# Kernel tuning notes

Hardware: AMD Instinct MI355X
Metric: run time of the kernel (lower is better)

## Reference

```python
import jax, jax.numpy as jnp
from jax import lax
import numpy as np

D_IN = 12      # latent_dim / flow input_dim
HALF = 6       # coupling split
HID = 192      # flow_hidden_dim
LAYERS = 24    # flow_layers
N_BASES = 66
SYM = 12       # symmetry_dim
OUT_DIM = 6    # rows of tangent frame J_p
B = 16384
EPS_P = 1e-3
CLAMP = 2.0    # soft clamp for 'exp_clamp' scale map: s = CLAMP*tanh(raw/CLAMP)


def _mlp(z1, p):
    W1, b1, W2, b2, W3, b3 = p
    h = jax.nn.relu(z1 @ W1.T + b1)
    h = jax.nn.relu(h @ W2.T + b2)
    return h @ W3.T + b3


def _coupling_fwd(z, p):
    # AffineCouplingBlock (split->affine->merge) followed by Permute(swap)
    z1, z2 = z[..., :HALF], z[..., HALF:]
    prm = _mlp(z1, p)
    shift, sraw = prm[..., 0::2], prm[..., 1::2]
    s = CLAMP * jnp.tanh(sraw / CLAMP)
    z2 = z2 * jnp.exp(s) + shift
    # merge [z1, z2'] then swap halves -> [z2', z1]
    return jnp.concatenate([z2, z1], axis=-1), jnp.sum(s, axis=-1)


def _coupling_inv(z, p):
    # inverse of Permute(swap) is swap again
    z = jnp.concatenate([z[..., HALF:], z[..., :HALF]], axis=-1)
    z1, z2 = z[..., :HALF], z[..., HALF:]
    prm = _mlp(z1, p)
    shift, sraw = prm[..., 0::2], prm[..., 1::2]
    s = CLAMP * jnp.tanh(sraw / CLAMP)
    z2 = (z2 - shift) * jnp.exp(-s)
    return jnp.concatenate([z1, z2], axis=-1), -jnp.sum(s, axis=-1)


def flow_forward(z, params):
    def step(c, p):
        z, ld = c
        z, d = _coupling_fwd(z, p)
        return (z, ld + d), None
    (z, ld), _ = lax.scan(step, (z, jnp.zeros(z.shape[:-1], z.dtype)), params)
    return z, ld


def flow_inverse(y, params):
    def step(c, p):
        z, ld = c
        z, d = _coupling_inv(z, p)
        return (z, ld + d), None
    (z, ld), _ = lax.scan(step, (y, jnp.zeros(y.shape[:-1], y.dtype)), params, reverse=True)
    return z, ld


def pullback_tangent(z, v, params):
    # J[b] = v[b] @ d(flow_forward)/dz at z[b], via per-sample vjp
    def one(zb, vb):
        _, vjp_fn = jax.vjp(lambda zz: flow_forward(zz, params)[0], zb)
        return jax.vmap(lambda r: vjp_fn(r)[0])(vb)
    return jax.vmap(one)(z, v)


def kl_divergence(J_p, J_q, log_var_diag):
    b, out_dim, in_dim = J_p.shape
    J_p = J_p / jnp.sqrt(jnp.sum(J_p * J_p))  # global normalization
    S_p = jnp.einsum('bni,bmi->bnm', J_p, J_p)
    S_q = jnp.einsum('bin,bim->bnm', J_q, J_q)
    S_pq = jnp.einsum('bni,bmi->bnm', J_p[:, :, :SYM], J_q)
    D = jnp.exp(-log_var_diag)  # (in_dim,)
    I_p = jnp.eye(out_dim, dtype=J_p.dtype)
    I_q = jnp.eye(SYM, dtype=J_q.dtype)
    M = S_p + EPS_P * I_p
    H = S_q + D[:SYM] * I_q
    norm_M = jnp.maximum(jnp.mean(jnp.diagonal(M, axis1=-2, axis2=-1), -1), 1e-6)
    norm_H = jnp.maximum(jnp.mean(jnp.diagonal(H, axis1=-2, axis2=-1), -1), 1e-6)
    M = M + 1e-3 * norm_M[:, None, None] * I_p
    H = H + 1e-3 * norm_H[:, None, None] * I_q
    Db = D + 1e-3 * norm_H[:, None]  # (b, in_dim)
    trace_p = jnp.einsum('bij,bij,bj->b', J_p, J_p, Db)
    trace_q = jnp.einsum('bij,bij->b', J_q, J_q)
    trace_pq = jnp.einsum('bij,bij->b', S_pq, S_pq)
    trace = (EPS_P + 1e-3 * norm_M) * (jnp.sum(Db, -1) + trace_q) + trace_p + trace_pq
    L_M = jnp.linalg.cholesky(M)
    L_H = jnp.linalg.cholesky(H)
    logdet_M = 2.0 * jnp.sum(jnp.log(jnp.diagonal(L_M, axis1=-2, axis2=-1)), -1)
    logdet_H = 2.0 * jnp.sum(jnp.log(jnp.diagonal(L_H, axis1=-2, axis2=-1)), -1)
    logdet_p = logdet_M + (in_dim - out_dim) * np.float32(np.log(EPS_P))
    logdet_q = logdet_H + jnp.sum(jnp.log(Db[:, SYM:]), -1)
    logdet = -(logdet_p + logdet_q)
    return 0.5 * (trace + logdet - in_dim)


def setup_inputs() -> dict:
    key = jax.random.key(0)
    ks = jax.random.split(key, 10)
    y = jax.random.normal(ks[0], (B, D_IN), jnp.float32)
    J_p = jax.random.normal(ks[1], (B, OUT_DIM, D_IN), jnp.float32)
    sc = 0.05
    W1 = sc * jax.random.normal(ks[2], (LAYERS, HID, HALF), jnp.float32)
    b1 = sc * jax.random.normal(ks[3], (LAYERS, HID), jnp.float32)
    W2 = sc * jax.random.normal(ks[4], (LAYERS, HID, HID), jnp.float32)
    b2 = sc * jax.random.normal(ks[5], (LAYERS, HID), jnp.float32)
    W3 = sc * jax.random.normal(ks[6], (LAYERS, D_IN, HID), jnp.float32)
    b3 = sc * jax.random.normal(ks[7], (LAYERS, D_IN), jnp.float32)
    Wsym = (1.0 / np.sqrt(SYM)) * jax.random.normal(ks[8], (N_BASES, SYM, SYM), jnp.float32)
    log_var_diag = jnp.zeros((D_IN,), jnp.float32)
    return {"y": y, "J_p": J_p, "W1": W1, "b1": b1, "W2": W2, "b2": b2,
            "W3": W3, "b3": b3, "Wsym": Wsym, "log_var_diag": log_var_diag}


def reference(y, J_p, W1, b1, W2, b2, W3, b3, Wsym, log_var_diag):
    params = (W1, b1, W2, b2, W3, b3)
    z, ld = flow_inverse(y, params)
    # DiagGaussian(trainable=False) base log prob = standard normal
    log_prob = ld - 0.5 * D_IN * np.float32(np.log(2.0 * np.pi)) - 0.5 * jnp.sum(z * z, -1)
    Jp = pullback_tangent(z, J_p, params)
    A = Wsym - jnp.swapaxes(Wsym, -1, -2)
    J_q = jnp.einsum('bi,mji->bmj', z[:, :SYM], A)
    kl = kl_divergence(Jp, J_q, log_var_diag)
    return (log_prob, kl)
```

## Files before the change

### kernel.cpp

```cpp
#include <hip/hip_runtime.h>
#include <hip/hip_bf16.h>
#include <math.h>

#define BTOT   16384
#define NLAYER 24
#define NDIN   12
#define HID    192
#define NBASE  66
#define EPSP   1e-3f
#define EPB    16

#define EST 200
#define W3ST 12
#define OB_H1  0
#define OB_G   6400
#define OB_R   44800
#define OB_W1  49408
#define OB_W3F 51712
#define OB_PRM 60928
#define OB_GZ  61696
#define OB_ZAB 64000
#define OB_ES  65536
#define OB_LD  65920
#define OB_ZQ  65984
#define OB_RED 66048
#define SMEM_BYTES 66080

typedef __attribute__((ext_vector_type(8))) short s8v;
typedef __attribute__((ext_vector_type(4))) float f4v;
#define MFMA16(a,b,c) __builtin_amdgcn_mfma_f32_16x16x32_bf16(a,b,c,0,0,0)

__device__ __forceinline__ unsigned short f2bf(float f) {
  unsigned u = __builtin_bit_cast(unsigned, f);
  u += 0x7fffu + ((u >> 16) & 1u);
  return (unsigned short)(u >> 16);
}
__device__ __forceinline__ float bf2f(unsigned short h) {
  unsigned u = ((unsigned)h) << 16;
  return __builtin_bit_cast(float, u);
}
__device__ __forceinline__ unsigned pk2(float a, float b) {
  return (unsigned)f2bf(a) | ((unsigned)f2bf(b) << 16);
}
__device__ __forceinline__ float blo(unsigned u) { return bf2f((unsigned short)(u & 0xffff)); }
__device__ __forceinline__ float bhi(unsigned u) { return bf2f((unsigned short)(u >> 16)); }

__global__ void prep_kernel(const float* __restrict__ W2,
                            unsigned short* __restrict__ w2b,
                            unsigned short* __restrict__ w2t) {
  int idx = blockIdx.x * 256 + threadIdx.x;
  int l   = idx / (HID * HID);
  int rem = idx - l * HID * HID;
  int k   = rem / HID;
  int j   = rem - k * HID;
  w2b[idx] = f2bf(W2[idx]);
  w2t[idx] = f2bf(W2[l * HID * HID + j * HID + k]);
}

__global__ __launch_bounds__(256) void flow_kernel(
    float* __restrict__ yz, float* __restrict__ jp,
    const float* __restrict__ W1, const float* __restrict__ b1,
    const float* __restrict__ b2,
    const float* __restrict__ W3, const float* __restrict__ b3,
    const unsigned short* __restrict__ w2b,
    const unsigned short* __restrict__ w2t,
    float* __restrict__ ws_sum, float* __restrict__ out_lp) {
  extern __shared__ char smraw[];
  unsigned short* sH1b = (unsigned short*)(smraw + OB_H1);
  unsigned short* sGb  = (unsigned short*)(smraw + OB_G);
  float* sW3f = (float*)(smraw + OB_W3F);
  float* sR   = (float*)(smraw + OB_R);
  float* cur  = (float*)(smraw + OB_PRM);
  float* sGZ  = (float*)(smraw + OB_GZ);
  float* sZA  = (float*)(smraw + OB_ZAB);
  float* sZB  = sZA + 192;
  float* sES  = (float*)(smraw + OB_ES);
  float* sLD  = (float*)(smraw + OB_LD);
  float* sZQ  = (float*)(smraw + OB_ZQ);
  float* sRed = (float*)(smraw + OB_RED);

  const int tid  = threadIdx.x;
  const int lane = tid & 63;
  const int w    = __builtin_amdgcn_readfirstlane(tid >> 6);
  const int e    = tid & 15;
  const int grp  = tid >> 4;
  const int lm   = lane & 15, lq = lane >> 4;
  const int blk  = blockIdx.x;

  if (tid < 96) {
    int i = tid >> 4;
    sZA[96 + i * 16 + e] = yz[(blk * EPB + e) * 12 + i];
    sZB[96 + i * 16 + e] = yz[(blk * EPB + e) * 12 + 6 + i];
  }
  if (tid < 16) { sLD[tid] = 0.f; sZQ[tid] = 0.f; }
  if (tid == 0) sRed[0] = 0.f;
  for (int idx = tid; idx < 576; idx += 256) sGZ[idx] = 0.f;
  for (int idx = tid; idx < 72 * EPB; idx += 256) {
    int rt = idx >> 4, ee = idx & 15;
    sR[idx] = jp[(blk * EPB + ee) * 72 + rt];
  }
  __syncthreads();

  for (int l = NLAYER - 1; l >= 0; --l) {
    const float* W1l = W1 + l * HID * 6;
    const float* b1l = b1 + l * HID;
    const float* b2l = b2 + l * HID;
    const float* W3l = W3 + l * NDIN * HID;
    const float* b3l = b3 + l * NDIN;
    const unsigned short* w2bl = w2b + l * HID * HID;
    const unsigned short* w2tl = w2t + l * HID * HID;
    const int p = l & 1;

    if (tid < 192) {
      const float* wr = W1l + tid * 6;
      unsigned* dst = (unsigned*)(smraw + OB_W1 + tid * 12);
      dst[0] = pk2(wr[0], wr[1]);
      dst[1] = pk2(wr[2], wr[3]);
      dst[2] = pk2(wr[4], wr[5]);
    }
    for (int idx = tid; idx < 2304; idx += 256) {
      int t = idx / 192, j = idx - t * 192;
      sW3f[j * W3ST + t] = W3l[idx];
    }
    if (tid < 192) cur[tid] = 0.f;
    if (l != NLAYER - 1) {
      for (int idx = tid; idx < 576; idx += 256) {
        int i = idx / 96, rem = idx - i * 96;
        int r = rem >> 4, e5 = rem & 15;
        float r1  = sR[(r * 12 + i) * EPB + e5];
        float r2o = sR[(r * 12 + 6 + i) * EPB + e5];
        float es  = sES[i * 16 + e5];
        sR[(r * 12 + i) * EPB + e5]     = r2o + sGZ[i * 96 + rem];
        sR[(r * 12 + 6 + i) * EPB + e5] = r1 * es;
        sGZ[i * 96 + rem] = 0.f;
      }
    }
    {
      float z1v[6];
      #pragma unroll
      for (int i = 0; i < 6; ++i) z1v[i] = sZB[p * 96 + i * 16 + e];
      #pragma unroll
      for (int ch = 0; ch < 2; ++ch) {
        int j0 = grp * 12 + ch * 6;
        float hv[6];
        #pragma unroll
        for (int jj = 0; jj < 6; ++jj) {
          int j = j0 + jj;
          float acc = b1l[j];
          #pragma unroll
          for (int i = 0; i < 6; ++i) acc = fmaf(W1l[j * 6 + i], z1v[i], acc);
          hv[jj] = fmaxf(acc, 0.f);
        }
        unsigned* dst = (unsigned*)&sH1b[e * EST + j0];
        dst[0] = pk2(hv[0], hv[1]);
        dst[1] = pk2(hv[2], hv[3]);
        dst[2] = pk2(hv[4], hv[5]);
      }
    }
    __syncthreads();

    {
      f4v acc2[3] = {{0,0,0,0},{0,0,0,0},{0,0,0,0}};
      #pragma unroll 2
      for (int kk = 0; kk < 6; ++kk) {
        int jo = kk * 32 + lq * 8;
        s8v Bv = *(const s8v*)&sH1b[lm * EST + jo];
        #pragma unroll
        for (int s = 0; s < 3; ++s) {
          s8v A = *(const s8v*)(w2bl + ((w + s * 4) * 16 + lm) * HID + jo);
          acc2[s] = MFMA16(A, Bv, acc2[s]);
        }
      }
      #pragma unroll
      for (int s = 0; s < 3; ++s) {
        int jb2 = (w + s * 4) * 16 + lq * 4;
        float hv[4];
        #pragma unroll
        for (int rg = 0; rg < 4; ++rg)
          hv[rg] = fmaxf(acc2[s][rg] + b2l[jb2 + rg], 0.f);
        unsigned* dst = (unsigned*)sGb + ((lm * EST + jb2) >> 1);
        dst[0] = pk2(hv[0], hv[1]);
        dst[1] = pk2(hv[2], hv[3]);
        float pp[12];
        #pragma unroll
        for (int t = 0; t < 12; ++t) pp[t] = 0.f;
        #pragma unroll
        for (int rg = 0; rg < 4; ++rg) {
          const float* w3r = sW3f + (jb2 + rg) * W3ST;
          float v = hv[rg];
          #pragma unroll
          for (int t = 0; t < 12; ++t) pp[t] = fmaf(w3r[t], v, pp[t]);
        }
        #pragma unroll
        for (int t = 0; t < 12; ++t) {
          float v = pp[t];
          v += __shfl_xor(v, 16);
          v += __shfl_xor(v, 32);
          if (lane < 16) atomicAdd(&cur[t * EPB + lane], v);
        }
      }
    }
    __syncthreads();

    {
      unsigned mbits = 0;
      {
        const unsigned* hp = (const unsigned*)&sGb[e * EST + grp * 12];
        #pragma unroll
        for (int c = 0; c < 6; ++c) {
          unsigned m = hp[c];
          mbits |= ((m & 0xffffu) ? 1u : 0u) << (2 * c);
          mbits |= ((m >> 16)     ? 1u : 0u) << (2 * c + 1);
        }
      }
      float tf[6];
      #pragma unroll
      for (int c = 0; c < 6; ++c) {
        float sh = b3l[2 * c]     + cur[(2 * c) * EPB + e];
        float sr = b3l[2 * c + 1] + cur[(2 * c + 1) * EPB + e];
        float s  = 2.f * tanhf(0.5f * sr);
        float tv = sZA[p * 96 + c * 16 + e] - sh;
        tf[c] = tv * (1.f - 0.25f * s * s);
        if (tid < 96 && (tid >> 4) == c) {
          sZA[(p ^ 1) * 96 + c * 16 + e] = sZB[p * 96 + c * 16 + e];
          sZB[(p ^ 1) * 96 + c * 16 + e] = tv * expf(-s);
          sES[c * 16 + e] = expf(s);
          atomicAdd(&sLD[e], -s);
        }
      }
      float r1[6][6];
      #pragma unroll
      for (int r = 0; r < 6; ++r)
        #pragma unroll
        for (int c = 0; c < 6; ++c)
          r1[r][c] = sR[(r * 12 + c) * EPB + e];
      #pragma unroll
      for (int ch = 0; ch < 2; ++ch) {
        int j0 = grp * 12 + ch * 6;
        #pragma unroll
        for (int pr = 0; pr < 3; ++pr) {
          const float* wp0 = sW3f + (j0 + 2 * pr)     * W3ST;
          const float* wp1 = sW3f + (j0 + 2 * pr + 1) * W3ST;
          float wc0[6], wc1[6];
          #pragma unroll
          for (int c = 0; c < 6; ++c) {
            wc0[c] = fmaf(tf[c], wp0[2 * c + 1], wp0[2 * c]);
            wc1[c] = fmaf(tf[c], wp1[2 * c + 1], wp1[2 * c]);
          }
          unsigned b0 = (mbits >> (ch * 6 + 2 * pr))     & 1u;
          unsigned b1 = (mbits >> (ch * 6 + 2 * pr + 1)) & 1u;
          #pragma unroll
          for (int r = 0; r < 6; ++r) {
            float a0 = 0.f, a1 = 0.f;
            #pragma unroll
            for (int c = 0; c < 6; ++c) {
              a0 = fmaf(wc0[c], r1[r][c], a0);
              a1 = fmaf(wc1[c], r1[r][c], a1);
            }
            *(unsigned*)&sGb[(r * 16 + e) * EST + j0 + 2 * pr] =
                pk2(b0 ? a0 : 0.f, b1 ? a1 : 0.f);
          }
        }
      }
    }
    __syncthreads();

    {
      const int mtg = w * 3;
      #pragma unroll 1
      for (int nc = 0; nc < 2; ++nc) {
        f4v acc[3][3] = {{{0,0,0,0},{0,0,0,0},{0,0,0,0}},
                         {{0,0,0,0},{0,0,0,0},{0,0,0,0}},
                         {{0,0,0,0},{0,0,0,0},{0,0,0,0}}};
        #pragma unroll 2
        for (int kk = 0; kk < 6; ++kk) {
          int jo = kk * 32 + lq * 8;
          s8v A[3], Bv[3];
          #pragma unroll
          for (int pq = 0; pq < 3; ++pq)
            A[pq] = *(const s8v*)(w2tl + ((mtg + pq) * 16 + lm) * HID + jo);
          #pragma unroll
          for (int q = 0; q < 3; ++q)
            Bv[q] = *(const s8v*)&sGb[((nc * 3 + q) * 16 + lm) * EST + jo];
          #pragma unroll
          for (int pq = 0; pq < 3; ++pq)
            #pragma unroll
            for (int q = 0; q < 3; ++q)
              acc[pq][q] = MFMA16(A[pq], Bv[q], acc[pq][q]);
        }
        float pz[3][6];
        #pragma unroll
        for (int q = 0; q < 3; ++q)
          #pragma unroll
          for (int i = 0; i < 6; ++i) pz[q][i] = 0.f;
        #pragma unroll
        for (int pq = 0; pq < 3; ++pq) {
          int kb = (mtg + pq) * 16 + lq * 4;
          const unsigned* mp = (const unsigned*)&sH1b[lm * EST + kb];
          unsigned mm0 = mp[0], mm1 = mp[1];
          #pragma unroll
          for (int rg = 0; rg < 4; ++rg) {
            const unsigned* wp =
                (const unsigned*)(smraw + OB_W1 + (kb + rg) * 12);
            unsigned wx = wp[0], wy = wp[1], wz = wp[2];
            float w0 = blo(wx), w1c = bhi(wx), w2c = blo(wy);
            float w3c = bhi(wy), w4c = blo(wz), w5c = bhi(wz);
            unsigned mm = (rg >> 1) ? mm1 : mm0;
            unsigned short hb = (rg & 1) ? (unsigned short)(mm >> 16)
                                         : (unsigned short)(mm & 0xffffu);
            #pragma unroll
            for (int q = 0; q < 3; ++q) {
              float val = hb ? acc[pq][q][rg] : 0.f;
              pz[q][0] = fmaf(w0, val, pz[q][0]);
              pz[q][1] = fmaf(w1c, val, pz[q][1]);
              pz[q][2] = fmaf(w2c, val, pz[q][2]);
              pz[q][3] = fmaf(w3c, val, pz[q][3]);
              pz[q][4] = fmaf(w4c, val, pz[q][4]);
              pz[q][5] = fmaf(w5c, val, pz[q][5]);
            }
          }
        }
        #pragma unroll
        for (int q = 0; q < 3; ++q)
          #pragma unroll
          for (int i = 0; i < 6; ++i) {
            float v = pz[q][i];
            v += __shfl_xor(v, 16);
            v += __shfl_xor(v, 32);
            if (lane < 16)
              atomicAdd(&sGZ[i * 96 + (nc * 3 + q) * 16 + lane], v);
          }
      }
    }
    __syncthreads();
  }

  {
    for (int idx = tid; idx < 576; idx += 256) {
      int i = idx / 96, rem = idx - i * 96;
      int r = rem >> 4, e5 = rem & 15;
      float r1  = sR[(r * 12 + i) * EPB + e5];
      float r2o = sR[(r * 12 + 6 + i) * EPB + e5];
      float es  = sES[i * 16 + e5];
      sR[(r * 12 + i) * EPB + e5]     = r2o + sGZ[i * 96 + rem];
      sR[(r * 12 + 6 + i) * EPB + e5] = r1 * es;
    }
  }
  if (tid < 96) {
    int i = tid >> 4;
    float zaf = sZA[96 + i * 16 + e];
    float zbf = sZB[96 + i * 16 + e];
    yz[(blk * EPB + e) * 12 + i]     = zaf;
    yz[(blk * EPB + e) * 12 + 6 + i] = zbf;
    atomicAdd(&sZQ[e], fmaf(zaf, zaf, zbf * zbf));
  }
  __syncthreads();
  if (tid < 16)
    out_lp[blk * EPB + tid] = sLD[tid] - 11.027262398456072f - 0.5f * sZQ[tid];

  float part = 0.f;
  for (int idx = tid; idx < 72 * EPB; idx += 256) {
    int rt = idx >> 4, ee = idx & 15;
    float v = sR[idx];
    jp[(blk * EPB + ee) * 72 + rt] = v;
    part = fmaf(v, v, part);
  }
  #pragma unroll
  for (int off = 32; off > 0; off >>= 1) part += __shfl_down(part, off, 64);
  if ((tid & 63) == 0) atomicAdd(&sRed[0], part);
  __syncthreads();
  if (tid == 0) atomicAdd(ws_sum, sRed[0]);
}

__global__ __launch_bounds__(256) void kl_kernel(
    const float* __restrict__ zin, const float* __restrict__ jpin,
    const float* __restrict__ Wsym, const float* __restrict__ lvd,
    const float* __restrict__ ws_sum, float* __restrict__ out_kl) {
  int elem = blockIdx.x * 256 + threadIdx.x;
  float z[12];
  #pragma unroll
  for (int i = 0; i < 12; ++i) z[i] = zin[elem * 12 + i];
  float scale = 1.0f / sqrtf(ws_sum[0]);
  float Jp[6][12];
  #pragma unroll
  for (int n = 0; n < 6; ++n)
    #pragma unroll
    for (int j = 0; j < 12; ++j)
      Jp[n][j] = jpin[elem * 72 + n * 12 + j] * scale;

  float Sq[78];
  #pragma unroll
  for (int i = 0; i < 78; ++i) Sq[i] = 0.f;
  float tq = 0.f, tpq = 0.f;

  for (int m = 0; m < NBASE; ++m) {
    const float* Wm = Wsym + m * 144;
    float jq[12];
    #pragma unroll
    for (int j = 0; j < 12; ++j) {
      float acc = 0.f;
      #pragma unroll
      for (int i = 0; i < 12; ++i)
        acc = fmaf(Wm[j * 12 + i] - Wm[i * 12 + j], z[i], acc);
      jq[j] = acc;
    }
    #pragma unroll
    for (int i = 0; i < 12; ++i) {
      tq = fmaf(jq[i], jq[i], tq);
      #pragma unroll
      for (int j = 0; j <= i; ++j)
        Sq[i * (i + 1) / 2 + j] = fmaf(jq[i], jq[j], Sq[i * (i + 1) / 2 + j]);
    }
    #pragma unroll
    for (int n = 0; n < 6; ++n) {
      float d = 0.f;
      #pragma unroll
      for (int j = 0; j < 12; ++j) d = fmaf(Jp[n][j], jq[j], d);
      tpq = fmaf(d, d, tpq);
    }
  }

  float Dv[12], Db[12];
  #pragma unroll
  for (int j = 0; j < 12; ++j) Dv[j] = expf(-lvd[j]);

  float mh = 0.f;
  #pragma unroll
  for (int i = 0; i < 12; ++i) mh += Sq[i * (i + 1) / 2 + i] + Dv[i];
  float norm_H = fmaxf(mh * (1.f / 12.f), 1e-6f);
  #pragma unroll
  for (int i = 0; i < 12; ++i) Sq[i * (i + 1) / 2 + i] += Dv[i] + 1e-3f * norm_H;
  float sumDb = 0.f;
  #pragma unroll
  for (int j = 0; j < 12; ++j) { Db[j] = Dv[j] + 1e-3f * norm_H; sumDb += Db[j]; }

  float M[21];
  #pragma unroll
  for (int n = 0; n < 6; ++n)
    #pragma unroll
    for (int mm = 0; mm <= n; ++mm) {
      float acc = 0.f;
      #pragma unroll
      for (int j = 0; j < 12; ++j) acc = fmaf(Jp[n][j], Jp[mm][j], acc);
      M[n * (n + 1) / 2 + mm] = acc;
    }
  float md = 0.f;
  #pragma unroll
  for (int i = 0; i < 6; ++i) md += M[i * (i + 1) / 2 + i];
  float norm_M = fmaxf(md * (1.f / 6.f) + EPSP, 1e-6f);
  #pragma unroll
  for (int i = 0; i < 6; ++i) M[i * (i + 1) / 2 + i] += EPSP + 1e-3f * norm_M;

  float trace_p = 0.f;
  #pragma unroll
  for (int n = 0; n < 6; ++n)
    #pragma unroll
    for (int j = 0; j < 12; ++j)
      trace_p = fmaf(Jp[n][j] * Jp[n][j], Db[j], trace_p);

  float trace = (EPSP + 1e-3f * norm_M) * (sumDb + tq) + trace_p + tpq;

  float ldM = 0.f;
  #pragma unroll
  for (int jc = 0; jc < 6; ++jc) {
    float d = M[jc * (jc + 1) / 2 + jc];
    #pragma unroll
    for (int k = 0; k < jc; ++k) d -= M[jc * (jc + 1) / 2 + k] * M[jc * (jc + 1) / 2 + k];
    d = sqrtf(d);
    ldM += logf(d);
    float di = 1.f / d;
    M[jc * (jc + 1) / 2 + jc] = d;
    #pragma unroll
    for (int i2 = jc + 1; i2 < 6; ++i2) {
      float v = M[i2 * (i2 + 1) / 2 + jc];
      #pragma unroll
      for (int k = 0; k < jc; ++k) v -= M[i2 * (i2 + 1) / 2 + k] * M[jc * (jc + 1) / 2 + k];
      M[i2 * (i2 + 1) / 2 + jc] = v * di;
    }
  }

  float ldH = 0.f;
  #pragma unroll
  for (int jc = 0; jc < 12; ++jc) {
    float d = Sq[jc * (jc + 1) / 2 + jc];
    #pragma unroll
    for (int k = 0; k < jc; ++k) d -= Sq[jc * (jc + 1) / 2 + k] * Sq[jc * (jc + 1) / 2 + k];
    d = sqrtf(d);
    ldH += logf(d);
    float di = 1.f / d;
    Sq[jc * (jc + 1) / 2 + jc] = d;
    #pragma unroll
    for (int i2 = jc + 1; i2 < 12; ++i2) {
      float v = Sq[i2 * (i2 + 1) / 2 + jc];
      #pragma unroll
      for (int k = 0; k < jc; ++k) v -= Sq[i2 * (i2 + 1) / 2 + k] * Sq[jc * (jc + 1) / 2 + k];
      Sq[i2 * (i2 + 1) / 2 + jc] = v * di;
    }
  }

  float logdet_p = 2.f * ldM + 6.f * logf(EPSP);
  float logdet_q = 2.f * ldH;
  out_kl[elem] = 0.5f * (trace - (logdet_p + logdet_q) - 12.f);
}

extern "C" void kernel_launch(void* const* d_in, const int* in_sizes, int n_in,
                              void* d_out, int out_size, void* d_ws, size_t ws_size,
                              hipStream_t stream) {
  (void)in_sizes; (void)n_in; (void)out_size; (void)ws_size;
  float* y    = (float*)d_in[0];
  float* Jp   = (float*)d_in[1];
  const float* W1   = (const float*)d_in[2];
  const float* b1   = (const float*)d_in[3];
  const float* W2   = (const float*)d_in[4];
  const float* b2   = (const float*)d_in[5];
  const float* W3   = (const float*)d_in[6];
  const float* b3   = (const float*)d_in[7];
  const float* Wsym = (const float*)d_in[8];
  const float* lvd  = (const float*)d_in[9];
  float* out = (float*)d_out;

  float* ws_sum = (float*)d_ws;
  unsigned short* w2b = (unsigned short*)((char*)d_ws + 256);
  unsigned short* w2t = (unsigned short*)((char*)d_ws + 256 +
                                          NLAYER * HID * HID * 2);
  hipMemsetAsync(d_ws, 0, 4, stream);

  hipFuncSetAttribute((const void*)flow_kernel,
                      hipFuncAttributeMaxDynamicSharedMemorySize, SMEM_BYTES);

  prep_kernel<<<3456, 256, 0, stream>>>(W2, w2b, w2t);
  flow_kernel<<<BTOT / EPB, 256, SMEM_BYTES, stream>>>(
      y, Jp, W1, b1, b2, W3, b3, w2b, w2t, ws_sum, out);
  kl_kernel<<<64, 256, 0, stream>>>(y, Jp, Wsym, lvd, ws_sum, out + BTOT);
}
```

Measured before the change: 1.621 ms.

## Split KL basis loop across four lanes per element with shared antisymmetric Wsym

```diff
diff --git a/kernel.cpp b/kernel.cpp
--- a/kernel.cpp
+++ b/kernel.cpp
@@ -376,7 +376,18 @@
     const float* __restrict__ zin, const float* __restrict__ jpin,
     const float* __restrict__ Wsym, const float* __restrict__ lvd,
     const float* __restrict__ ws_sum, float* __restrict__ out_kl) {
-  int elem = blockIdx.x * 256 + threadIdx.x;
+  __shared__ float sA[NBASE * 144];
+  const int tid   = threadIdx.x;
+  const int elem  = (blockIdx.x * 256 + tid) >> 2;
+  const int slice = tid & 3;
+
+  for (int idx = tid; idx < NBASE * 144; idx += 256) {
+    int m = idx / 144, r = idx - m * 144;
+    int j = r / 12, i = r - j * 12;
+    sA[idx] = Wsym[m * 144 + j * 12 + i] - Wsym[m * 144 + i * 12 + j];
+  }
+  __syncthreads();
+
   float z[12];
   #pragma unroll
   for (int i = 0; i < 12; ++i) z[i] = zin[elem * 12 + i];
@@ -393,15 +404,17 @@
   for (int i = 0; i < 78; ++i) Sq[i] = 0.f;
   float tq = 0.f, tpq = 0.f;
 
-  for (int m = 0; m < NBASE; ++m) {
-    const float* Wm = Wsym + m * 144;
+  const int m0 = (slice < 2) ? slice * 17 : 34 + (slice - 2) * 16;
+  const int m1 = m0 + ((slice < 2) ? 17 : 16);
+  for (int m = m0; m < m1; ++m) {
+    const float* Am = sA + m * 144;
     float jq[12];
     #pragma unroll
     for (int j = 0; j < 12; ++j) {
       float acc = 0.f;
       #pragma unroll
       for (int i = 0; i < 12; ++i)
-        acc = fmaf(Wm[j * 12 + i] - Wm[i * 12 + j], z[i], acc);
+        acc = fmaf(Am[j * 12 + i], z[i], acc);
       jq[j] = acc;
     }
     #pragma unroll
@@ -419,6 +432,16 @@
       tpq = fmaf(d, d, tpq);
     }
   }
+
+  #pragma unroll
+  for (int i = 0; i < 78; ++i) {
+    float v = Sq[i];
+    v += __shfl_xor(v, 1);
+    v += __shfl_xor(v, 2);
+    Sq[i] = v;
+  }
+  tq  += __shfl_xor(tq, 1);  tq  += __shfl_xor(tq, 2);
+  tpq += __shfl_xor(tpq, 1); tpq += __shfl_xor(tpq, 2);
 
   float Dv[12], Db[12];
   #pragma unroll
@@ -500,7 +523,8 @@
 
   float logdet_p = 2.f * ldM + 6.f * logf(EPSP);
   float logdet_q = 2.f * ldH;
-  out_kl[elem] = 0.5f * (trace - (logdet_p + logdet_q) - 12.f);
+  if (slice == 0)
+    out_kl[elem] = 0.5f * (trace - (logdet_p + logdet_q) - 12.f);
 }
 
 extern "C" void kernel_launch(void* const* d_in, const int* in_sizes, int n_in,
@@ -531,5 +555,6 @@
   prep_kernel<<<3456, 256, 0, stream>>>(W2, w2b, w2t);
   flow_kernel<<<BTOT / EPB, 256, SMEM_BYTES, stream>>>(
       y, Jp, W1, b1, b2, W3, b3, w2b, w2t, ws_sum, out);
-  kl_kernel<<<64, 256, 0, stream>>>(y, Jp, Wsym, lvd, ws_sum, out + BTOT);
-}
+  kl_kernel<<<BTOT * 4 / 256, 256, 0, stream>>>(y, Jp, Wsym, lvd, ws_sum,
+                                                out + BTOT);
+}
```

After: 1.482 ms. 8.6% less time.
